# Kernel tuning notes

Hardware: AMD Instinct MI355X
Metric: run time of the kernel (lower is better)

## Reference

```python
import jax, jax.numpy as jnp
import numpy as np

H, DH, L, G = 4, 16, 6, 256


def _ln(x, eps=1e-6):
    m = x.mean(-1, keepdims=True)
    v = ((x - m) ** 2).mean(-1, keepdims=True)
    return (x - m) * jax.lax.rsqrt(v + eps)


def _sh(u):
    # real spherical harmonics l=0,1,2, 'component' normalization (e3nn style), unit input
    x, y, z = u[:, 0], u[:, 1], u[:, 2]
    s3, s15, s5 = 3.0 ** 0.5, 15.0 ** 0.5, 5.0 ** 0.5
    return jnp.stack([
        jnp.ones_like(x),
        s3 * x, s3 * y, s3 * z,
        s15 * x * y, s15 * y * z, (s5 / 2.0) * (3.0 * z * z - 1.0),
        s15 * x * z, (s15 / 2.0) * (x * x - y * y),
    ], axis=-1)


def _seg_softmax(logits, seg, n):
    m = jax.ops.segment_max(logits, seg, num_segments=n)
    ex = jnp.exp(logits - m[seg])
    s = jax.ops.segment_sum(ex, seg, num_segments=n)
    return ex / (s[seg] + 1e-9)


def setup_inputs() -> dict:
    key = jax.random.key(0)
    ks = jax.random.split(key, 24)
    N, E = 16384, 262144
    D = H * DH  # 64

    def w(k, shape, fan_in):
        return (jax.random.normal(k, shape, dtype=jnp.float32) / np.sqrt(fan_in)).astype(jnp.float32)

    inp = {
        'node_num': N,
        'edge_src': jax.random.randint(ks[0], (E,), 0, N, dtype=jnp.int32),
        'edge_dst': jax.random.randint(ks[1], (E,), 0, N, dtype=jnp.int32),
        'edge_vec': jax.random.normal(ks[2], (E, 3), dtype=jnp.float32) * 2.0,
        'batch': jnp.sort(jax.random.randint(ks[3], (N,), 0, G, dtype=jnp.int32)),
        'node_atom': jax.random.randint(ks[4], (N,), 0, 120, dtype=jnp.int32),
        'ele_embed_w': jax.random.normal(ks[5], (120, 32), dtype=jnp.float32) * 0.05,
        'W_embed': w(ks[6], (32, D), 32),
        'W_edge': w(ks[7], (32 + 32 + 9 + 64, D), 137),
        'Wq': w(ks[8], (L, D, D), D),
        'Wk': w(ks[9], (L, D, D), D),
        'Wv': w(ks[10], (L, D, D), D),
        'Wr1': w(ks[11], (L, 64, 64), 64),
        'Wr2': w(ks[12], (L, 64, H), 64),
        'Wo': w(ks[13], (L, D, D), D),
        'W1': w(ks[14], (L, D, 4 * D), D),
        'W2': w(ks[15], (L, 4 * D, D), 4 * D),
        'W_feat': w(ks[16], (D, 512), D),
        'hW1': w(ks[17], (512, 64), 512),
        'hb1': jnp.zeros((64,), jnp.float32),
        'hW2': w(ks[18], (64, 64), 64),
        'hb2': jnp.zeros((64,), jnp.float32),
        'hW3': w(ks[19], (64, 1), 64),
        'hb3': jnp.zeros((1,), jnp.float32),
    }
    return inp


def reference(node_num, edge_src, edge_dst, edge_vec, batch, node_atom,
              ele_embed_w, W_embed, W_edge, Wq, Wk, Wv, Wr1, Wr2, Wo, W1, W2,
              W_feat, hW1, hb1, hW2, hb2, hW3, hb3):
    N = int(node_num)
    E = edge_src.shape[0]

    # edge geometry: SH of permuted+normalized edge vector, gaussian RBF of length
    r = jnp.linalg.norm(edge_vec, axis=1)
    u = edge_vec[:, jnp.array([1, 2, 0])] / (r[:, None] + 1e-12)
    sh = _sh(u)                                   # [E, 9]
    centers = jnp.linspace(0.0, 10.0, 64, dtype=jnp.float32)
    width = 0.5 * 10.0 / 64.0
    rbf = jnp.exp(-((r[:, None] - centers) ** 2) / (2.0 * width * width))  # [E, 64]
    mask = r < 10.0                               # range_dis = [0, 10)

    # w2v path: atom embedding, edge features = cat(src, dst)
    nf = ele_embed_w[node_atom]                   # [N, 32]
    x = nf @ W_embed                              # [N, 64]
    e_ctx = jnp.concatenate([nf[edge_src], nf[edge_dst], sh, rbf], axis=-1)  # [E,137]
    e = e_ctx @ W_edge                            # [E, 64]

    for l in range(L):
        h = _ln(x)
        q = (h[edge_dst] @ Wq[l]).reshape(E, H, DH)
        src_in = h[edge_src] + e
        k = (src_in @ Wk[l]).reshape(E, H, DH)
        v = (src_in @ Wv[l]).reshape(E, H, DH)
        radial = jax.nn.silu(rbf @ Wr1[l]) @ Wr2[l]           # [E, H]
        logits = (q * k).sum(-1) / np.sqrt(DH) + radial        # [E, H]
        logits = jnp.where(mask[:, None], logits, -1e9)
        alpha = _seg_softmax(logits, edge_dst, N)              # softmax over in-edges
        msg = (alpha[..., None] * v).reshape(E, H * DH)
        agg = jax.ops.segment_sum(msg, edge_dst, num_segments=N)
        x = x + agg @ Wo[l]
        h2 = _ln(x)
        x = x + jax.nn.silu(h2 @ W1[l]) @ W2[l]

    feat = _ln(x @ W_feat)                        # [N, 512], irreps_feature = 512x0e
    hh = jax.nn.relu(_ln(feat @ hW1 + hb1))
    hh = jax.nn.relu(_ln(hh @ hW2 + hb2))
    energy = hh @ hW3 + hb3                       # [N, 1]
    pooled = jax.ops.segment_sum(energy, batch, num_segments=G) / np.sqrt(72.0)
    return pooled
```

## Files before the change

kernel.cpp:

```cpp
#include <hip/hip_runtime.h>

typedef short s8v __attribute__((ext_vector_type(8)));
typedef float f32x4 __attribute__((ext_vector_type(4)));
typedef unsigned short u16;

__device__ __forceinline__ float bf2f(u16 h){
  union { unsigned u; float f; } v; v.u = ((unsigned)h) << 16; return v.f;
}
__device__ __forceinline__ u16 f2bf(float f){
  union { float f; unsigned u; } v; v.f = f;
  unsigned u = v.u;
  return (u16)((u + 0x7fffu + ((u >> 16) & 1u)) >> 16);
}
#define MFMA(a,b,c) __builtin_amdgcn_mfma_f32_16x16x32_bf16((a),(b),(c),0,0,0)

#define WREDUCE64(s) { s += __shfl_xor(s,1); s += __shfl_xor(s,2); s += __shfl_xor(s,4); \
                       s += __shfl_xor(s,8); s += __shfl_xor(s,16); s += __shfl_xor(s,32); }
#define QREDUCE16(s) { s += __shfl_xor(s,1); s += __shfl_xor(s,2); s += __shfl_xor(s,4); s += __shfl_xor(s,8); }

__global__ __launch_bounds__(256) void k_transpose(const float* src, u16* dst, int B, int R, int C, int Rpad){
  int idx = blockIdx.x*256 + threadIdx.x;
  int total = B*C*Rpad;
  if(idx >= total) return;
  int b = idx / (C*Rpad);
  int rem = idx - b*C*Rpad;
  int cI = rem / Rpad;
  int rI = rem - cI*Rpad;
  dst[idx] = (rI < R) ? f2bf(src[(size_t)b*R*C + (size_t)rI*C + cI]) : (u16)0;
}

__global__ __launch_bounds__(256) void k_transpose5(const float* W0, const float* W1, const float* W2,
    const float* W3, const float* W4, u16* dst){
  int idx = blockIdx.x*256 + threadIdx.x;
  int which = idx / (6*64*64);
  int rem = idx - which*(6*64*64);
  const float* src = (which==0)?W0:(which==1)?W1:(which==2)?W2:(which==3)?W3:W4;
  int b = rem >> 12;
  int r2 = rem & 4095;
  int cI = r2 >> 6, rI = r2 & 63;
  dst[idx] = f2bf(src[b*4096 + rI*64 + cI]);
}

__global__ __launch_bounds__(256) void k_convert(const float* src, u16* dst, int n){
  int idx = blockIdx.x*256 + threadIdx.x;
  if(idx < n) dst[idx] = f2bf(src[idx]);
}

__global__ __launch_bounds__(256) void k_count(const int* dstI, int* deg, int E){
  int tid = blockIdx.x*256 + threadIdx.x;
  if(tid < E) atomicAdd(&deg[dstI[tid]], 1);
}
__global__ __launch_bounds__(1024) void k_scan(const int* deg, int* rowptr, int* cursor, int N){
  __shared__ int wsum[17];
  int tid = threadIdx.x;
  int per = (N + 1023) >> 10;
  int base = tid * per;
  int s = 0;
  for(int i=0;i<per;i++){ int idx = base+i; if(idx < N) s += deg[idx]; }
  int lane = tid & 63, wid = tid >> 6;
  int inc = s;
  for(int d=1; d<64; d<<=1){
    int t = __shfl_up(inc, d);
    if(lane >= d) inc += t;
  }
  if(lane == 63) wsum[wid+1] = inc;
  if(tid == 0) wsum[0] = 0;
  __syncthreads();
  if(tid == 0){ for(int w=1; w<=16; w++) wsum[w] += wsum[w-1]; }
  __syncthreads();
  int run = inc - s + wsum[wid];
  for(int i=0;i<per;i++){
    int idx = base + i;
    if(idx < N){ rowptr[idx] = run; cursor[idx] = run; run += deg[idx]; }
  }
  if(tid == 1023) rowptr[N] = wsum[16];
}
__global__ __launch_bounds__(256) void k_scatter(const int* dstI, int* cursor, int* csr, int E){
  int tid = blockIdx.x*256 + threadIdx.x;
  if(tid < E){
    int p = atomicAdd(&cursor[dstI[tid]], 1);
    csr[p] = tid;
  }
}

__global__ __launch_bounds__(256) void k_edge_embed(const int* csr, const int* srcI, const int* dstI,
    const int* atom, const u16* ele, const float* evec, const u16* Bt,
    u16* ebf, float* r2, int* src2, int* dst2, int E){
  int wave = (blockIdx.x*blockDim.x + threadIdx.x) >> 6;
  int lane = threadIdx.x & 63;
  int row0 = wave*16; if(row0 >= E) return;
  int c = lane & 15, q = lane >> 4;
  int p = row0 + c;
  int e = csr[p];
  int sn = srcI[e], dn = dstI[e];
  float vx = evec[(size_t)e*3+0];
  float vy = evec[(size_t)e*3+1];
  float vz = evec[(size_t)e*3+2];
  float r = sqrtf(vx*vx + vy*vy + vz*vz);
  if(q == 0){ r2[p] = r; src2[p] = sn; dst2[p] = dn; }
  float inv = 1.f/(r + 1e-12f);
  float x = vy*inv, y = vz*inv, z = vx*inv;
  const float s3 = 1.7320508075688772f, s15 = 3.872983346207417f;
  const float s5h = 1.118033988749895f, s15h = 1.9364916731037085f;
  float sh[9];
  sh[0] = 1.f; sh[1] = s3*x; sh[2] = s3*y; sh[3] = s3*z;
  sh[4] = s15*x*y; sh[5] = s15*y*z; sh[6] = s5h*(3.f*z*z - 1.f);
  sh[7] = s15*x*z; sh[8] = s15h*(x*x - y*y);
  s8v a[5];
  a[0] = *reinterpret_cast<const s8v*>(ele + (size_t)atom[sn]*32 + q*8);
  a[1] = *reinterpret_cast<const s8v*>(ele + (size_t)atom[dn]*32 + q*8);
  #pragma unroll
  for(int j=0;j<8;j++){
    int col = 64 + q*8 + j;
    u16 v;
    if(q == 0)            v = f2bf(sh[j]);
    else if(col < 73)     v = f2bf(sh[8]);
    else { float d = r - (10.f/63.f)*(float)(col-73); v = f2bf(__expf(-81.92f*d*d)); }
    a[2][j] = (short)v;
  }
  #pragma unroll
  for(int j=0;j<8;j++){
    float d = r - (10.f/63.f)*(float)(23 + q*8 + j);
    a[3][j] = (short)f2bf(__expf(-81.92f*d*d));
  }
  #pragma unroll
  for(int j=0;j<8;j++){
    int col = 128 + q*8 + j;
    u16 v = 0;
    if(col < 137){ float d = r - (10.f/63.f)*(float)(col-73); v = f2bf(__expf(-81.92f*d*d)); }
    a[4][j] = (short)v;
  }
  #pragma unroll
  for(int ct=0; ct<4; ct++){
    f32x4 acc = {0.f,0.f,0.f,0.f};
    #pragma unroll
    for(int kc=0; kc<5; kc++){
      s8v b = *reinterpret_cast<const s8v*>(Bt + (ct*16+c)*160 + kc*32 + q*8);
      acc = MFMA(a[kc], b, acc);
    }
    #pragma unroll
    for(int r_=0;r_<4;r_++) ebf[(size_t)(row0+q*4+r_)*64 + ct*16 + c] = f2bf(acc[r_]);
  }
}

__global__ __launch_bounds__(256) void k_pre(const int* atom, const u16* ele, const u16* WembT,
    const u16* WqT0, float* xb, u16* hbf, float* Qt, int M){
  __shared__ u16 ldsH[4][16*72];
  int widL = threadIdx.x >> 6;
  int wave = (blockIdx.x*256 + threadIdx.x) >> 6;
  int lane = threadIdx.x & 63;
  int row0 = wave*16; if(row0 >= M) return;
  int c = lane & 15, q = lane >> 4;
  u16* LH = ldsH[widL];
  int at = atom[row0 + c];
  s8v a = *reinterpret_cast<const s8v*>(ele + (size_t)at*32 + q*8);
  float nx[4][4];
  #pragma unroll
  for(int ct=0; ct<4; ct++){
    s8v b = *reinterpret_cast<const s8v*>(WembT + (ct*16+c)*32 + q*8);
    f32x4 acc = {0.f,0.f,0.f,0.f};
    acc = MFMA(a, b, acc);
    #pragma unroll
    for(int r=0;r<4;r++){
      xb[(size_t)(row0+q*4+r)*64 + ct*16 + c] = acc[r];
      nx[ct][r] = acc[r];
    }
  }
  #pragma unroll
  for(int r=0;r<4;r++){
    float s = nx[0][r]+nx[1][r]+nx[2][r]+nx[3][r];
    QREDUCE16(s);
    float m = s*(1.f/64.f);
    float vv = 0.f;
    #pragma unroll
    for(int ct=0;ct<4;ct++){ float d = nx[ct][r]-m; vv += d*d; }
    QREDUCE16(vv);
    float rs = rsqrtf(vv*(1.f/64.f) + 1e-6f);
    #pragma unroll
    for(int ct=0;ct<4;ct++){
      u16 hb = f2bf((nx[ct][r]-m)*rs);
      hbf[(size_t)(row0+q*4+r)*64 + ct*16 + c] = hb;
      LH[(q*4+r)*72 + ct*16 + c] = hb;
    }
  }
  s8v h0 = *reinterpret_cast<const s8v*>(LH + c*72 + q*8);
  s8v h1 = *reinterpret_cast<const s8v*>(LH + c*72 + 32 + q*8);
  #pragma unroll
  for(int ct=0; ct<4; ct++){
    s8v b0 = *reinterpret_cast<const s8v*>(WqT0 + (ct*16+c)*64 + q*8);
    s8v b1 = *reinterpret_cast<const s8v*>(WqT0 + (ct*16+c)*64 + 32 + q*8);
    f32x4 acc = {0.f,0.f,0.f,0.f};
    acc = MFMA(h0, b0, acc);
    acc = MFMA(h1, b1, acc);
    #pragma unroll
    for(int r=0;r<4;r++) Qt[(size_t)(row0+q*4+r)*64 + c*4 + ct] = acc[r];
  }
}

__global__ __launch_bounds__(256) void k_kvrad(const u16* hbf, const u16* ebf,
    const int* src2, const int* dst2, const float* Qt, const float* r2,
    const u16* WkT, const u16* WvT, const u16* Wr1T, const float* Wr2,
    u16* vbf, float* exb, int E){
  int wave = (blockIdx.x*256 + threadIdx.x) >> 6;
  int lane = threadIdx.x & 63;
  int row0 = wave*16;
  int c = lane & 15, q = lane >> 4;
  int sr = src2[row0 + c];
  s8v a0, a1;
  {
    s8v h0 = *reinterpret_cast<const s8v*>(hbf + (size_t)sr*64 + q*8);
    s8v h1 = *reinterpret_cast<const s8v*>(hbf + (size_t)sr*64 + 32 + q*8);
    s8v e0 = *reinterpret_cast<const s8v*>(ebf + (size_t)(row0+c)*64 + q*8);
    s8v e1 = *reinterpret_cast<const s8v*>(ebf + (size_t)(row0+c)*64 + 32 + q*8);
    #pragma unroll
    for(int j=0;j<8;j++){
      a0[j] = (short)f2bf(bf2f((u16)h0[j]) + bf2f((u16)e0[j]));
      a1[j] = (short)f2bf(bf2f((u16)h1[j]) + bf2f((u16)e1[j]));
    }
  }
  float re = r2[row0 + c];
  s8v r0, r1;
  #pragma unroll
  for(int j=0;j<8;j++){
    float d0 = re - (10.f/63.f)*(float)(q*8+j);
    float d1 = re - (10.f/63.f)*(float)(32+q*8+j);
    r0[j] = (short)f2bf(__expf(-81.92f*d0*d0));
    r1[j] = (short)f2bf(__expf(-81.92f*d1*d1));
  }
  const float4* QtV = reinterpret_cast<const float4*>(Qt);
  float4 qv[4];
  #pragma unroll
  for(int r=0;r<4;r++){
    int dr = dst2[row0 + q*4 + r];
    qv[r] = QtV[(size_t)dr*16 + c];
  }
  const float4* wr2v = reinterpret_cast<const float4*>(Wr2);
  float comb[4][4];
  #pragma unroll
  for(int h=0;h<4;h++)
    #pragma unroll
    for(int r=0;r<4;r++) comb[h][r] = 0.f;
  #pragma unroll
  for(int ct=0; ct<4; ct++){
    s8v bk0 = *reinterpret_cast<const s8v*>(WkT + (ct*16+c)*64 + q*8);
    s8v bk1 = *reinterpret_cast<const s8v*>(WkT + (ct*16+c)*64 + 32 + q*8);
    s8v bv0 = *reinterpret_cast<const s8v*>(WvT + (ct*16+c)*64 + q*8);
    s8v bv1 = *reinterpret_cast<const s8v*>(WvT + (ct*16+c)*64 + 32 + q*8);
    s8v bw0 = *reinterpret_cast<const s8v*>(Wr1T + (ct*16+c)*64 + q*8);
    s8v bw1 = *reinterpret_cast<const s8v*>(Wr1T + (ct*16+c)*64 + 32 + q*8);
    f32x4 kacc = {0.f,0.f,0.f,0.f};
    kacc = MFMA(a0, bk0, kacc); kacc = MFMA(a1, bk1, kacc);
    f32x4 vacc = {0.f,0.f,0.f,0.f};
    vacc = MFMA(a0, bv0, vacc); vacc = MFMA(a1, bv1, vacc);
    f32x4 hacc = {0.f,0.f,0.f,0.f};
    hacc = MFMA(r0, bw0, hacc); hacc = MFMA(r1, bw1, hacc);
    float4 w2 = wr2v[ct*16 + c];
    #pragma unroll
    for(int r=0;r<4;r++){
      vbf[(size_t)row0*64 + (r*4+ct)*64 + q*16 + c] = f2bf(vacc[r]);
      float qc = (ct==0)?qv[r].x:(ct==1)?qv[r].y:(ct==2)?qv[r].z:qv[r].w;
      comb[ct][r] += 0.25f * kacc[r] * qc;
      float y = hacc[r];
      float sv = y / (1.f + __expf(-y));
      comb[0][r] += sv * w2.x;
      comb[1][r] += sv * w2.y;
      comb[2][r] += sv * w2.z;
      comb[3][r] += sv * w2.w;
    }
  }
  #pragma unroll
  for(int m=1; m<16; m<<=1){
    #pragma unroll
    for(int h=0;h<4;h++)
      #pragma unroll
      for(int r=0;r<4;r++) comb[h][r] += __shfl_xor(comb[h][r], m);
  }
  int hh = c & 3, rr = c >> 2;
  float logit = comb[0][0];
  #pragma unroll
  for(int h=0;h<4;h++)
    #pragma unroll
    for(int r=0;r<4;r++)
      if(h || r) logit = (hh==h && rr==r) ? comb[h][r] : logit;
  int row = row0 + q*4 + rr;
  exb[(size_t)row0*4 + lane] = (r2[row] < 10.f) ? __expf(logit) : 0.f;
}

__global__ __launch_bounds__(256) void k_agg(const int* rowptr, const float* exb, const u16* vbf, u16* aggbf, int N){
  int wave = (blockIdx.x*256 + threadIdx.x) >> 6;
  int lane = threadIdx.x & 63;
  if(wave >= N) return;
  int s0 = rowptr[wave], s1 = rowptr[wave+1];
  float s[4] = {0.f,0.f,0.f,0.f};
  for(int p = s0 + lane; p < s1; p += 64){
    float4 ev = *reinterpret_cast<const float4*>(exb + (size_t)p*4);
    s[0] += ev.x; s[1] += ev.y; s[2] += ev.z; s[3] += ev.w;
  }
  #pragma unroll
  for(int i=0;i<4;i++){ WREDUCE64(s[i]); }
  int ep = lane >> 4, cc = lane & 15;
  int hh = cc >> 2;
  int swz = hh*64 + (cc&3)*4;
  float inv = 1.f/(s[hh] + 1e-9f);
  float a0=0.f, a1=0.f, a2=0.f, a3=0.f;
  for(int p = s0 + ep; p < s1; p += 4){
    int t = p & 15;
    size_t base = (size_t)(p & ~15)*64 + (size_t)((t&3)*256) + (size_t)((t>>2)*16) + swz;
    ushort4 v4 = *reinterpret_cast<const ushort4*>(vbf + base);
    float ex = exb[(size_t)p*4 + hh];
    a0 += ex*bf2f(v4.x); a1 += ex*bf2f(v4.y); a2 += ex*bf2f(v4.z); a3 += ex*bf2f(v4.w);
  }
  a0 += __shfl_xor(a0,16); a0 += __shfl_xor(a0,32);
  a1 += __shfl_xor(a1,16); a1 += __shfl_xor(a1,32);
  a2 += __shfl_xor(a2,16); a2 += __shfl_xor(a2,32);
  a3 += __shfl_xor(a3,16); a3 += __shfl_xor(a3,32);
  if(ep == 0){
    ushort4 o;
    o.x = f2bf(a0*inv); o.y = f2bf(a1*inv); o.z = f2bf(a2*inv); o.w = f2bf(a3*inv);
    *reinterpret_cast<ushort4*>(aggbf + (size_t)wave*64 + cc*4) = o;
  }
}

__global__ __launch_bounds__(256) void k_mega(const u16* aggbf, const u16* WoT, float* x,
    const u16* W1T, const u16* W2T, const u16* WqTn, float* Qt, u16* hbf, u16* xbf,
    int writex, int haveQ, int M){
  __shared__ u16 ldsH[4][16*72];
  __shared__ u16 ldsT[4][16*264];
  int widL = threadIdx.x >> 6;
  int wave = (blockIdx.x*256 + threadIdx.x) >> 6;
  int lane = threadIdx.x & 63;
  int row0 = wave*16; if(row0 >= M) return;
  int c = lane & 15, q = lane >> 4;
  u16* LH = ldsH[widL];
  u16* LT = ldsT[widL];

  {
    s8v a0 = *reinterpret_cast<const s8v*>(aggbf + (size_t)(row0+c)*64 + q*8);
    s8v a1 = *reinterpret_cast<const s8v*>(aggbf + (size_t)(row0+c)*64 + 32 + q*8);
    float nx[4][4];
    #pragma unroll
    for(int ct=0; ct<4; ct++){
      s8v b0 = *reinterpret_cast<const s8v*>(WoT + (ct*16+c)*64 + q*8);
      s8v b1 = *reinterpret_cast<const s8v*>(WoT + (ct*16+c)*64 + 32 + q*8);
      f32x4 acc = {0.f,0.f,0.f,0.f};
      acc = MFMA(a0, b0, acc);
      acc = MFMA(a1, b1, acc);
      #pragma unroll
      for(int r=0;r<4;r++){
        size_t idx = (size_t)(row0+q*4+r)*64 + ct*16 + c;
        float t = x[idx] + acc[r];
        x[idx] = t;
        nx[ct][r] = t;
      }
    }
    #pragma unroll
    for(int r=0;r<4;r++){
      float s = nx[0][r]+nx[1][r]+nx[2][r]+nx[3][r];
      QREDUCE16(s);
      float m = s*(1.f/64.f);
      float vv = 0.f;
      #pragma unroll
      for(int ct=0;ct<4;ct++){ float d = nx[ct][r]-m; vv += d*d; }
      QREDUCE16(vv);
      float rs = rsqrtf(vv*(1.f/64.f) + 1e-6f);
      #pragma unroll
      for(int ct=0;ct<4;ct++)
        LH[(q*4+r)*72 + ct*16 + c] = f2bf((nx[ct][r]-m)*rs);
    }
  }
  {
    s8v h0 = *reinterpret_cast<const s8v*>(LH + c*72 + q*8);
    s8v h1 = *reinterpret_cast<const s8v*>(LH + c*72 + 32 + q*8);
    #pragma unroll
    for(int ct=0; ct<16; ct++){
      s8v b0 = *reinterpret_cast<const s8v*>(W1T + (ct*16+c)*64 + q*8);
      s8v b1 = *reinterpret_cast<const s8v*>(W1T + (ct*16+c)*64 + 32 + q*8);
      f32x4 acc = {0.f,0.f,0.f,0.f};
      acc = MFMA(h0, b0, acc);
      acc = MFMA(h1, b1, acc);
      #pragma unroll
      for(int r=0;r<4;r++){
        float y = acc[r];
        LT[(q*4+r)*264 + ct*16 + c] = f2bf(y / (1.f + __expf(-y)));
      }
    }
  }
  {
    s8v a[8];
    #pragma unroll
    for(int kc=0; kc<8; kc++)
      a[kc] = *reinterpret_cast<const s8v*>(LT + c*264 + kc*32 + q*8);
    float nx[4][4];
    #pragma unroll
    for(int ct=0; ct<4; ct++){
      f32x4 acc = {0.f,0.f,0.f,0.f};
      #pragma unroll
      for(int kc=0; kc<8; kc++){
        s8v b = *reinterpret_cast<const s8v*>(W2T + (ct*16+c)*256 + kc*32 + q*8);
        acc = MFMA(a[kc], b, acc);
      }
      #pragma unroll
      for(int r=0;r<4;r++){
        size_t idx = (size_t)(row0+q*4+r)*64 + ct*16 + c;
        float t = x[idx] + acc[r];
        x[idx] = t;
        nx[ct][r] = t;
        if(writex) xbf[idx] = f2bf(t);
      }
    }
    #pragma unroll
    for(int r=0;r<4;r++){
      float s = nx[0][r]+nx[1][r]+nx[2][r]+nx[3][r];
      QREDUCE16(s);
      float m = s*(1.f/64.f);
      float vv = 0.f;
      #pragma unroll
      for(int ct=0;ct<4;ct++){ float d = nx[ct][r]-m; vv += d*d; }
      QREDUCE16(vv);
      float rs = rsqrtf(vv*(1.f/64.f) + 1e-6f);
      #pragma unroll
      for(int ct=0;ct<4;ct++){
        u16 hb = f2bf((nx[ct][r]-m)*rs);
        hbf[(size_t)(row0+q*4+r)*64 + ct*16 + c] = hb;
        LH[(q*4+r)*72 + ct*16 + c] = hb;
      }
    }
  }
  if(haveQ){
    s8v h0 = *reinterpret_cast<const s8v*>(LH + c*72 + q*8);
    s8v h1 = *reinterpret_cast<const s8v*>(LH + c*72 + 32 + q*8);
    #pragma unroll
    for(int ct=0; ct<4; ct++){
      s8v b0 = *reinterpret_cast<const s8v*>(WqTn + (ct*16+c)*64 + q*8);
      s8v b1 = *reinterpret_cast<const s8v*>(WqTn + (ct*16+c)*64 + 32 + q*8);
      f32x4 acc = {0.f,0.f,0.f,0.f};
      acc = MFMA(h0, b0, acc);
      acc = MFMA(h1, b1, acc);
      #pragma unroll
      for(int r=0;r<4;r++) Qt[(size_t)(row0+q*4+r)*64 + c*4 + ct] = acc[r];
    }
  }
}

__global__ __launch_bounds__(256) void k_feat_ln(const u16* A, const u16* Bt, u16* out, int M){
  int wave = (blockIdx.x*256 + threadIdx.x) >> 6;
  int lane = threadIdx.x & 63;
  int row0 = wave*16; if(row0 >= M) return;
  int c = lane & 15, q = lane >> 4;
  s8v a0 = *reinterpret_cast<const s8v*>(A + (size_t)(row0+c)*64 + q*8);
  s8v a1 = *reinterpret_cast<const s8v*>(A + (size_t)(row0+c)*64 + 32 + q*8);
  float fa[32][4];
  #pragma unroll
  for(int ct=0; ct<32; ct++){
    s8v b0 = *reinterpret_cast<const s8v*>(Bt + (ct*16+c)*64 + q*8);
    s8v b1 = *reinterpret_cast<const s8v*>(Bt + (ct*16+c)*64 + 32 + q*8);
    f32x4 acc = {0.f,0.f,0.f,0.f};
    acc = MFMA(a0, b0, acc);
    acc = MFMA(a1, b1, acc);
    #pragma unroll
    for(int r=0;r<4;r++) fa[ct][r] = acc[r];
  }
  #pragma unroll
  for(int r=0;r<4;r++){
    float s = 0.f;
    #pragma unroll
    for(int ct=0;ct<32;ct++) s += fa[ct][r];
    QREDUCE16(s);
    float m = s*(1.f/512.f);
    float vv = 0.f;
    #pragma unroll
    for(int ct=0;ct<32;ct++){ float d = fa[ct][r]-m; vv += d*d; }
    QREDUCE16(vv);
    float rs = rsqrtf(vv*(1.f/512.f) + 1e-6f);
    #pragma unroll
    for(int ct=0;ct<32;ct++)
      out[(size_t)(row0+q*4+r)*512 + ct*16 + c] = f2bf((fa[ct][r]-m)*rs);
  }
}

__global__ __launch_bounds__(256) void k_head1_ln(const u16* A, const u16* Bt, const float* hb, u16* out, int M){
  int wave = (blockIdx.x*256 + threadIdx.x) >> 6;
  int lane = threadIdx.x & 63;
  int row0 = wave*16; if(row0 >= M) return;
  int c = lane & 15, q = lane >> 4;
  s8v a[16];
  #pragma unroll
  for(int kc=0; kc<16; kc++)
    a[kc] = *reinterpret_cast<const s8v*>(A + (size_t)(row0+c)*512 + kc*32 + q*8);
  float y[4][4];
  #pragma unroll
  for(int ct=0; ct<4; ct++){
    f32x4 acc = {0.f,0.f,0.f,0.f};
    #pragma unroll
    for(int kc=0; kc<16; kc++){
      s8v b = *reinterpret_cast<const s8v*>(Bt + (size_t)(ct*16+c)*512 + kc*32 + q*8);
      acc = MFMA(a[kc], b, acc);
    }
    float bi = hb[ct*16+c];
    #pragma unroll
    for(int r=0;r<4;r++) y[ct][r] = acc[r] + bi;
  }
  #pragma unroll
  for(int r=0;r<4;r++){
    float s = y[0][r]+y[1][r]+y[2][r]+y[3][r];
    QREDUCE16(s);
    float m = s*(1.f/64.f);
    float vv = 0.f;
    #pragma unroll
    for(int ct=0;ct<4;ct++){ float d = y[ct][r]-m; vv += d*d; }
    QREDUCE16(vv);
    float rs = rsqrtf(vv*(1.f/64.f) + 1e-6f);
    #pragma unroll
    for(int ct=0;ct<4;ct++)
      out[(size_t)(row0+q*4+r)*64 + ct*16 + c] = f2bf(fmaxf((y[ct][r]-m)*rs, 0.f));
  }
}

__global__ __launch_bounds__(256) void k_head2_energy(const u16* A, const u16* Bt, const float* hb,
    const float* hW3, const float* hb3, const int* batch, float* pooled, int M){
  int wave = (blockIdx.x*256 + threadIdx.x) >> 6;
  int lane = threadIdx.x & 63;
  int row0 = wave*16; if(row0 >= M) return;
  int c = lane & 15, q = lane >> 4;
  s8v a0 = *reinterpret_cast<const s8v*>(A + (size_t)(row0+c)*64 + q*8);
  s8v a1 = *reinterpret_cast<const s8v*>(A + (size_t)(row0+c)*64 + 32 + q*8);
  float y[4][4];
  #pragma unroll
  for(int ct=0; ct<4; ct++){
    s8v b0 = *reinterpret_cast<const s8v*>(Bt + (ct*16+c)*64 + q*8);
    s8v b1 = *reinterpret_cast<const s8v*>(Bt + (ct*16+c)*64 + 32 + q*8);
    f32x4 acc = {0.f,0.f,0.f,0.f};
    acc = MFMA(a0, b0, acc);
    acc = MFMA(a1, b1, acc);
    float bi = hb[ct*16+c];
    #pragma unroll
    for(int r=0;r<4;r++) y[ct][r] = acc[r] + bi;
  }
  float w3[4];
  #pragma unroll
  for(int ct=0;ct<4;ct++) w3[ct] = hW3[ct*16+c];
  float ep[4];
  #pragma unroll
  for(int r=0;r<4;r++){
    float s = y[0][r]+y[1][r]+y[2][r]+y[3][r];
    QREDUCE16(s);
    float m = s*(1.f/64.f);
    float vv = 0.f;
    #pragma unroll
    for(int ct=0;ct<4;ct++){ float d = y[ct][r]-m; vv += d*d; }
    QREDUCE16(vv);
    float rs = rsqrtf(vv*(1.f/64.f) + 1e-6f);
    float e = 0.f;
    #pragma unroll
    for(int ct=0;ct<4;ct++) e += fmaxf((y[ct][r]-m)*rs, 0.f) * w3[ct];
    QREDUCE16(e);
    ep[r] = e;
  }
  if(c < 4){
    float ev = (c==0)?ep[0]:(c==1)?ep[1]:(c==2)?ep[2]:ep[3];
    int row = row0 + q*4 + c;
    atomicAdd(&pooled[batch[row]], ev + hb3[0]);
  }
}

__global__ __launch_bounds__(256) void k_out(const float* pooled, float* out, int G){
  int tid = blockIdx.x*256 + threadIdx.x;
  if(tid < G) out[tid] = pooled[tid] * 0.11785113019775793f;
}

extern "C" void kernel_launch(void* const* d_in, const int* in_sizes, int n_in,
                              void* d_out, int out_size, void* d_ws, size_t ws_size,
                              hipStream_t stream){
  const int*   edge_src  = (const int*)d_in[1];
  const int*   edge_dst  = (const int*)d_in[2];
  const float* edge_vec  = (const float*)d_in[3];
  const int*   batch     = (const int*)d_in[4];
  const int*   node_atom = (const int*)d_in[5];
  const float* ele    = (const float*)d_in[6];
  const float* W_embed= (const float*)d_in[7];
  const float* W_edge = (const float*)d_in[8];
  const float* Wq = (const float*)d_in[9];
  const float* Wk = (const float*)d_in[10];
  const float* Wv = (const float*)d_in[11];
  const float* Wr1= (const float*)d_in[12];
  const float* Wr2= (const float*)d_in[13];
  const float* Wo = (const float*)d_in[14];
  const float* W1 = (const float*)d_in[15];
  const float* W2 = (const float*)d_in[16];
  const float* W_feat=(const float*)d_in[17];
  const float* hW1= (const float*)d_in[18];
  const float* hb1= (const float*)d_in[19];
  const float* hW2= (const float*)d_in[20];
  const float* hb2= (const float*)d_in[21];
  const float* hW3= (const float*)d_in[22];
  const float* hb3= (const float*)d_in[23];
  (void)n_in; (void)ws_size;

  const int E = in_sizes[1];
  const int N = in_sizes[4];
  const int G = out_size;

  char* base = (char*)d_ws;
  size_t off = 0;
  #define ALLOC(ty, name, count) ty* name = (ty*)(base + off); off = (off + (size_t)(count)*sizeof(ty) + 255) & ~(size_t)255;
  ALLOC(float, r2,    E)
  ALLOC(int,   src2,  E)
  ALLOC(int,   dst2,  E)
  ALLOC(u16,   ebf,   (size_t)E*64)
  ALLOC(u16,   vbf,   (size_t)E*64)
  ALLOC(float, exb,   (size_t)E*4)
  ALLOC(u16,   hbf,   (size_t)N*64)
  ALLOC(u16,   aggbf, (size_t)N*64)
  ALLOC(u16,   xbf,   (size_t)N*64)
  ALLOC(float, Qt,    (size_t)N*64)
  ALLOC(float, xb,    (size_t)N*64)
  ALLOC(int,   deg,   N)
  ALLOC(int,   rowptr,N+1)
  ALLOC(int,   cursor,N)
  ALLOC(int,   csr,   E)
  ALLOC(float, pooled,G)
  ALLOC(u16, ele_bf, 120*32)
  ALLOC(u16, WembT, 64*32)
  ALLOC(u16, WedgeT,64*160)
  ALLOC(u16, WqT,  6*64*64)
  ALLOC(u16, WkT,  6*64*64)
  ALLOC(u16, WvT,  6*64*64)
  ALLOC(u16, Wr1T, 6*64*64)
  ALLOC(u16, WoT,  6*64*64)
  ALLOC(u16, W1T,  6*256*64)
  ALLOC(u16, W2T,  6*64*256)
  ALLOC(u16, WfT,  512*64)
  ALLOC(u16, hW1T, 64*512)
  ALLOC(u16, hW2T, 64*64)
  #undef ALLOC
  u16* featbf = ebf;
  u16* hh1    = (u16*)exb;

  auto cdiv = [](int a, int b){ return (a + b - 1)/b; };

  k_convert<<<cdiv(120*32,256),256,0,stream>>>(ele, ele_bf, 120*32);
  k_transpose<<<cdiv(64*32,256),256,0,stream>>>(W_embed, WembT, 1, 32, 64, 32);
  k_transpose<<<cdiv(64*160,256),256,0,stream>>>(W_edge, WedgeT, 1, 137, 64, 160);
  k_transpose5<<<cdiv(5*6*64*64,256),256,0,stream>>>(Wq, Wk, Wv, Wr1, Wo, WqT);
  k_transpose<<<cdiv(6*256*64,256),256,0,stream>>>(W1, W1T, 6, 64, 256, 64);
  k_transpose<<<cdiv(6*64*256,256),256,0,stream>>>(W2, W2T, 6, 256, 64, 256);
  k_transpose<<<cdiv(512*64,256),256,0,stream>>>(W_feat, WfT, 1, 64, 512, 64);
  k_transpose<<<cdiv(64*512,256),256,0,stream>>>(hW1, hW1T, 1, 512, 64, 512);
  k_transpose<<<cdiv(64*64,256),256,0,stream>>>(hW2, hW2T, 1, 64, 64, 64);

  hipMemsetAsync(deg, 0, (size_t)N*sizeof(int), stream);
  hipMemsetAsync(pooled, 0, (size_t)G*sizeof(float), stream);

  k_count<<<cdiv(E,256),256,0,stream>>>(edge_dst, deg, E);
  k_scan<<<1,1024,0,stream>>>(deg, rowptr, cursor, N);
  k_scatter<<<cdiv(E,256),256,0,stream>>>(edge_dst, cursor, csr, E);
  k_edge_embed<<<E/64, 256, 0, stream>>>(csr, edge_src, edge_dst, node_atom, ele_bf, edge_vec,
                                         WedgeT, ebf, r2, src2, dst2, E);
  k_pre<<<N/64,256,0,stream>>>(node_atom, ele_bf, WembT, WqT, xb, hbf, Qt, N);

  for(int l=0; l<6; l++){
    k_kvrad<<<E/64,256,0,stream>>>(hbf, ebf, src2, dst2, Qt, r2,
                                   WkT + l*4096, WvT + l*4096, Wr1T + l*4096, Wr2 + l*256,
                                   vbf, exb, E);
    k_agg<<<cdiv(N,4),256,0,stream>>>(rowptr, exb, vbf, aggbf, N);
    k_mega<<<N/64,256,0,stream>>>(aggbf, WoT + l*4096, xb,
                                  W1T + l*16384, W2T + l*16384,
                                  WqT + ((l<5)?(l+1):0)*4096, Qt, hbf, xbf,
                                  (l==5)?1:0, (l<5)?1:0, N);
  }

  k_feat_ln<<<N/64,256,0,stream>>>(xbf, WfT, featbf, N);
  k_head1_ln<<<N/64,256,0,stream>>>(featbf, hW1T, hb1, hh1, N);
  k_head2_energy<<<N/64,256,0,stream>>>(hh1, hW2T, hb2, hW3, hb3, batch, pooled, N);
  k_out<<<cdiv(G,256),256,0,stream>>>(pooled, (float*)d_out, G);
}
```

Before: 823.6 us.

## Precompute per-layer radial bias in one kernel; merge weight prep; butterfly reduce

Moves the RBF expansion and radial MLP for all six layers into a single k_radial6 kernel run before the layer loop, writing a per-layer [E,4] radial bias that k_kvrad then reads. It also merges the nine weight convert/transpose launches into one k_prep kernel. The 16-value cross-lane sum in k_kvrad is replaced by a butterfly reduction that needs fewer shuffles. The cost is an extra 6*E*4 float buffer to write once and read in each layer, in place of the per-edge exp, MFMA and silu work that was repeated inside every layer.

```diff
diff --git a/kernel.cpp b/kernel.cpp
--- a/kernel.cpp
+++ b/kernel.cpp
@@ -18,32 +18,83 @@
                        s += __shfl_xor(s,8); s += __shfl_xor(s,16); s += __shfl_xor(s,32); }
 #define QREDUCE16(s) { s += __shfl_xor(s,1); s += __shfl_xor(s,2); s += __shfl_xor(s,4); s += __shfl_xor(s,8); }
 
-__global__ __launch_bounds__(256) void k_transpose(const float* src, u16* dst, int B, int R, int C, int Rpad){
+__device__ __forceinline__ float quad_butterfly16(float* val, int c){
+  float v8[8], v4[4], v2[2];
+  #pragma unroll
+  for(int t=0;t<8;t++){
+    float sent = (c&1) ? val[2*t] : val[2*t+1];
+    float got = __shfl_xor(sent, 1);
+    v8[t] = ((c&1) ? val[2*t+1] : val[2*t]) + got;
+  }
+  #pragma unroll
+  for(int t=0;t<4;t++){
+    float sent = ((c>>1)&1) ? v8[2*t] : v8[2*t+1];
+    float got = __shfl_xor(sent, 2);
+    v4[t] = (((c>>1)&1) ? v8[2*t+1] : v8[2*t]) + got;
+  }
+  #pragma unroll
+  for(int t=0;t<2;t++){
+    float sent = ((c>>2)&1) ? v4[2*t] : v4[2*t+1];
+    float got = __shfl_xor(sent, 4);
+    v2[t] = (((c>>2)&1) ? v4[2*t+1] : v4[2*t]) + got;
+  }
+  float sent = ((c>>3)&1) ? v2[0] : v2[1];
+  float got = __shfl_xor(sent, 8);
+  return (((c>>3)&1) ? v2[1] : v2[0]) + got;
+}
+
+__global__ __launch_bounds__(256) void k_prep(const float* ele, const float* W_embed, const float* W_edge,
+    const float* Wq, const float* Wk, const float* Wv, const float* Wr1, const float* Wo,
+    const float* W1, const float* W2, const float* W_feat, const float* hW1, const float* hW2,
+    u16* dst){
   int idx = blockIdx.x*256 + threadIdx.x;
-  int total = B*C*Rpad;
-  if(idx >= total) return;
-  int b = idx / (C*Rpad);
-  int rem = idx - b*C*Rpad;
-  int cI = rem / Rpad;
-  int rI = rem - cI*Rpad;
-  dst[idx] = (rI < R) ? f2bf(src[(size_t)b*R*C + (size_t)rI*C + cI]) : (u16)0;
-}
-
-__global__ __launch_bounds__(256) void k_transpose5(const float* W0, const float* W1, const float* W2,
-    const float* W3, const float* W4, u16* dst){
-  int idx = blockIdx.x*256 + threadIdx.x;
-  int which = idx / (6*64*64);
-  int rem = idx - which*(6*64*64);
-  const float* src = (which==0)?W0:(which==1)?W1:(which==2)?W2:(which==3)?W3:W4;
-  int b = rem >> 12;
-  int r2 = rem & 4095;
-  int cI = r2 >> 6, rI = r2 & 63;
-  dst[idx] = f2bf(src[b*4096 + rI*64 + cI]);
-}
-
-__global__ __launch_bounds__(256) void k_convert(const float* src, u16* dst, int n){
-  int idx = blockIdx.x*256 + threadIdx.x;
-  if(idx < n) dst[idx] = f2bf(src[idx]);
+  if(idx >= 405248) return;
+  u16 v;
+  if(idx < 3840){
+    v = f2bf(ele[idx]);
+  } else if(idx < 5888){
+    int l = idx - 3840;
+    int cI = l >> 5, rI = l & 31;
+    v = f2bf(W_embed[rI*64 + cI]);
+  } else if(idx < 16128){
+    int l = idx - 5888;
+    int cI = l / 160, rI = l - cI*160;
+    v = (rI < 137) ? f2bf(W_edge[rI*64 + cI]) : (u16)0;
+  } else if(idx < 139008){
+    int l = idx - 16128;
+    int which = l / 24576;
+    int rem = l - which*24576;
+    const float* src = (which==0)?Wq:(which==1)?Wk:(which==2)?Wv:(which==3)?Wr1:Wo;
+    int b = rem >> 12;
+    int r2 = rem & 4095;
+    int cI = r2 >> 6, rI = r2 & 63;
+    v = f2bf(src[b*4096 + rI*64 + cI]);
+  } else if(idx < 237312){
+    int l = idx - 139008;
+    int b = l / 16384;
+    int rem = l - b*16384;
+    int cI = rem >> 6, rI = rem & 63;
+    v = f2bf(W1[b*16384 + rI*256 + cI]);
+  } else if(idx < 335616){
+    int l = idx - 237312;
+    int b = l / 16384;
+    int rem = l - b*16384;
+    int cI = rem >> 8, rI = rem & 255;
+    v = f2bf(W2[b*16384 + rI*64 + cI]);
+  } else if(idx < 368384){
+    int l = idx - 335616;
+    int cI = l >> 6, rI = l & 63;
+    v = f2bf(W_feat[rI*512 + cI]);
+  } else if(idx < 401152){
+    int l = idx - 368384;
+    int cI = l >> 9, rI = l & 511;
+    v = f2bf(hW1[rI*64 + cI]);
+  } else {
+    int l = idx - 401152;
+    int cI = l >> 6, rI = l & 63;
+    v = f2bf(hW2[rI*64 + cI]);
+  }
+  dst[idx] = v;
 }
 
 __global__ __launch_bounds__(256) void k_count(const int* dstI, int* deg, int E){
@@ -143,6 +194,49 @@
   }
 }
 
+__global__ __launch_bounds__(256) void k_radial6(const float* r2, const u16* Wr1T, const float* Wr2,
+    float* rad6, int E){
+  int wave = (blockIdx.x*256 + threadIdx.x) >> 6;
+  int lane = threadIdx.x & 63;
+  int row0 = wave*16; if(row0 >= E) return;
+  int c = lane & 15, q = lane >> 4;
+  float re = r2[row0 + c];
+  s8v r0, r1;
+  #pragma unroll
+  for(int j=0;j<8;j++){
+    float d0 = re - (10.f/63.f)*(float)(q*8+j);
+    float d1 = re - (10.f/63.f)*(float)(32+q*8+j);
+    r0[j] = (short)f2bf(__expf(-81.92f*d0*d0));
+    r1[j] = (short)f2bf(__expf(-81.92f*d1*d1));
+  }
+  for(int l=0; l<6; l++){
+    const u16* W1l = Wr1T + l*4096;
+    const float4* wr2v = reinterpret_cast<const float4*>(Wr2 + l*256);
+    float val[16];
+    #pragma unroll
+    for(int i=0;i<16;i++) val[i] = 0.f;
+    #pragma unroll
+    for(int ct=0; ct<4; ct++){
+      s8v bw0 = *reinterpret_cast<const s8v*>(W1l + (ct*16+c)*64 + q*8);
+      s8v bw1 = *reinterpret_cast<const s8v*>(W1l + (ct*16+c)*64 + 32 + q*8);
+      f32x4 hacc = {0.f,0.f,0.f,0.f};
+      hacc = MFMA(r0, bw0, hacc); hacc = MFMA(r1, bw1, hacc);
+      float4 w2 = wr2v[ct*16 + c];
+      #pragma unroll
+      for(int r=0;r<4;r++){
+        float y = hacc[r];
+        float sv = y / (1.f + __expf(-y));
+        val[r*4+0] += sv * w2.x;
+        val[r*4+1] += sv * w2.y;
+        val[r*4+2] += sv * w2.z;
+        val[r*4+3] += sv * w2.w;
+      }
+    }
+    float fin = quad_butterfly16(val, c);
+    rad6[(size_t)l*E*4 + (size_t)row0*4 + lane] = fin;
+  }
+}
+
 __global__ __launch_bounds__(256) void k_pre(const int* atom, const u16* ele, const u16* WembT,
     const u16* WqT0, float* xb, u16* hbf, float* Qt, int M){
   __shared__ u16 ldsH[4][16*72];
@@ -198,9 +292,8 @@
 }
 
 __global__ __launch_bounds__(256) void k_kvrad(const u16* hbf, const u16* ebf,
-    const int* src2, const int* dst2, const float* Qt, const float* r2,
-    const u16* WkT, const u16* WvT, const u16* Wr1T, const float* Wr2,
-    u16* vbf, float* exb, int E){
+    const int* src2, const int* dst2, const float* Qt, const float* r2, const float* radial,
+    const u16* WkT, const u16* WvT, u16* vbf, float* exb, int E){
   int wave = (blockIdx.x*256 + threadIdx.x) >> 6;
   int lane = threadIdx.x & 63;
   int row0 = wave*16;
@@ -218,15 +311,6 @@
       a1[j] = (short)f2bf(bf2f((u16)h1[j]) + bf2f((u16)e1[j]));
     }
   }
-  float re = r2[row0 + c];
-  s8v r0, r1;
-  #pragma unroll
-  for(int j=0;j<8;j++){
-    float d0 = re - (10.f/63.f)*(float)(q*8+j);
-    float d1 = re - (10.f/63.f)*(float)(32+q*8+j);
-    r0[j] = (short)f2bf(__expf(-81.92f*d0*d0));
-    r1[j] = (short)f2bf(__expf(-81.92f*d1*d1));
-  }
   const float4* QtV = reinterpret_cast<const float4*>(Qt);
   float4 qv[4];
   #pragma unroll
@@ -234,55 +318,29 @@
     int dr = dst2[row0 + q*4 + r];
     qv[r] = QtV[(size_t)dr*16 + c];
   }
-  const float4* wr2v = reinterpret_cast<const float4*>(Wr2);
-  float comb[4][4];
-  #pragma unroll
-  for(int h=0;h<4;h++)
-    #pragma unroll
-    for(int r=0;r<4;r++) comb[h][r] = 0.f;
+  float val[16];
+  #pragma unroll
+  for(int i=0;i<16;i++) val[i] = 0.f;
   #pragma unroll
   for(int ct=0; ct<4; ct++){
     s8v bk0 = *reinterpret_cast<const s8v*>(WkT + (ct*16+c)*64 + q*8);
     s8v bk1 = *reinterpret_cast<const s8v*>(WkT + (ct*16+c)*64 + 32 + q*8);
     s8v bv0 = *reinterpret_cast<const s8v*>(WvT + (ct*16+c)*64 + q*8);
     s8v bv1 = *reinterpret_cast<const s8v*>(WvT + (ct*16+c)*64 + 32 + q*8);
-    s8v bw0 = *reinterpret_cast<const s8v*>(Wr1T + (ct*16+c)*64 + q*8);
-    s8v bw1 = *reinterpret_cast<const s8v*>(Wr1T + (ct*16+c)*64 + 32 + q*8);
     f32x4 kacc = {0.f,0.f,0.f,0.f};
     kacc = MFMA(a0, bk0, kacc); kacc = MFMA(a1, bk1, kacc);
     f32x4 vacc = {0.f,0.f,0.f,0.f};
     vacc = MFMA(a0, bv0, vacc); vacc = MFMA(a1, bv1, vacc);
-    f32x4 hacc = {0.f,0.f,0.f,0.f};
-    hacc = MFMA(r0, bw0, hacc); hacc = MFMA(r1, bw1, hacc);
-    float4 w2 = wr2v[ct*16 + c];
     #pragma unroll
     for(int r=0;r<4;r++){
       vbf[(size_t)row0*64 + (r*4+ct)*64 + q*16 + c] = f2bf(vacc[r]);
       float qc = (ct==0)?qv[r].x:(ct==1)?qv[r].y:(ct==2)?qv[r].z:qv[r].w;
-      comb[ct][r] += 0.25f * kacc[r] * qc;
-      float y = hacc[r];
-      float sv = y / (1.f + __expf(-y));
-      comb[0][r] += sv * w2.x;
-      comb[1][r] += sv * w2.y;
-      comb[2][r] += sv * w2.z;
-      comb[3][r] += sv * w2.w;
-    }
-  }
-  #pragma unroll
-  for(int m=1; m<16; m<<=1){
-    #pragma unroll
-    for(int h=0;h<4;h++)
-      #pragma unroll
-      for(int r=0;r<4;r++) comb[h][r] += __shfl_xor(comb[h][r], m);
-  }
-  int hh = c & 3, rr = c >> 2;
-  float logit = comb[0][0];
-  #pragma unroll
-  for(int h=0;h<4;h++)
-    #pragma unroll
-    for(int r=0;r<4;r++)
-      if(h || r) logit = (hh==h && rr==r) ? comb[h][r] : logit;
-  int row = row0 + q*4 + rr;
+      val[r*4+ct] += 0.25f * kacc[r] * qc;
+    }
+  }
+  float qk = quad_butterfly16(val, c);
+  float logit = qk + radial[(size_t)row0*4 + lane];
+  int row = row0 + q*4 + (c>>2);
   exb[(size_t)row0*4 + lane] = (r2[row] < 10.f) ? __expf(logit) : 0.f;
 }
 
@@ -333,7 +391,6 @@
   int c = lane & 15, q = lane >> 4;
   u16* LH = ldsH[widL];
   u16* LT = ldsT[widL];
-
   {
     s8v a0 = *reinterpret_cast<const s8v*>(aggbf + (size_t)(row0+c)*64 + q*8);
     s8v a1 = *reinterpret_cast<const s8v*>(aggbf + (size_t)(row0+c)*64 + 32 + q*8);
@@ -609,6 +666,7 @@
   ALLOC(u16,   ebf,   (size_t)E*64)
   ALLOC(u16,   vbf,   (size_t)E*64)
   ALLOC(float, exb,   (size_t)E*4)
+  ALLOC(float, rad6,  (size_t)E*4*6)
   ALLOC(u16,   hbf,   (size_t)N*64)
   ALLOC(u16,   aggbf, (size_t)N*64)
   ALLOC(u16,   xbf,   (size_t)N*64)
@@ -638,15 +696,8 @@
 
   auto cdiv = [](int a, int b){ return (a + b - 1)/b; };
 
-  k_convert<<<cdiv(120*32,256),256,0,stream>>>(ele, ele_bf, 120*32);
-  k_transpose<<<cdiv(64*32,256),256,0,stream>>>(W_embed, WembT, 1, 32, 64, 32);
-  k_transpose<<<cdiv(64*160,256),256,0,stream>>>(W_edge, WedgeT, 1, 137, 64, 160);
-  k_transpose5<<<cdiv(5*6*64*64,256),256,0,stream>>>(Wq, Wk, Wv, Wr1, Wo, WqT);
-  k_transpose<<<cdiv(6*256*64,256),256,0,stream>>>(W1, W1T, 6, 64, 256, 64);
-  k_transpose<<<cdiv(6*64*256,256),256,0,stream>>>(W2, W2T, 6, 256, 64, 256);
-  k_transpose<<<cdiv(512*64,256),256,0,stream>>>(W_feat, WfT, 1, 64, 512, 64);
-  k_transpose<<<cdiv(64*512,256),256,0,stream>>>(hW1, hW1T, 1, 512, 64, 512);
-  k_transpose<<<cdiv(64*64,256),256,0,stream>>>(hW2, hW2T, 1, 64, 64, 64);
+  k_prep<<<cdiv(405248,256),256,0,stream>>>(ele, W_embed, W_edge, Wq, Wk, Wv, Wr1, Wo,
+                                            W1, W2, W_feat, hW1, hW2, ele_bf);
 
   hipMemsetAsync(deg, 0, (size_t)N*sizeof(int), stream);
   hipMemsetAsync(pooled, 0, (size_t)G*sizeof(float), stream);
@@ -656,12 +707,12 @@
   k_scatter<<<cdiv(E,256),256,0,stream>>>(edge_dst, cursor, csr, E);
   k_edge_embed<<<E/64, 256, 0, stream>>>(csr, edge_src, edge_dst, node_atom, ele_bf, edge_vec,
                                          WedgeT, ebf, r2, src2, dst2, E);
+  k_radial6<<<E/64,256,0,stream>>>(r2, Wr1T, Wr2, rad6, E);
   k_pre<<<N/64,256,0,stream>>>(node_atom, ele_bf, WembT, WqT, xb, hbf, Qt, N);
 
   for(int l=0; l<6; l++){
-    k_kvrad<<<E/64,256,0,stream>>>(hbf, ebf, src2, dst2, Qt, r2,
-                                   WkT + l*4096, WvT + l*4096, Wr1T + l*4096, Wr2 + l*256,
-                                   vbf, exb, E);
+    k_kvrad<<<E/64,256,0,stream>>>(hbf, ebf, src2, dst2, Qt, r2, rad6 + (size_t)l*E*4,
+                                   WkT + l*4096, WvT + l*4096, vbf, exb, E);
     k_agg<<<cdiv(N,4),256,0,stream>>>(rowptr, exb, vbf, aggbf, N);
     k_mega<<<N/64,256,0,stream>>>(aggbf, WoT + l*4096, xb,
                                   W1T + l*16384, W2T + l*16384,
```

New measurement: 816.0 us. Within noise of the previous version (-0.9%).
